# Kernel optimization log

Hardware: AMD Instinct MI355X
Metric: run time of the kernel (lower is better)

## Reference

```python
import jax, jax.numpy as jnp
import numpy as np

B, T, D, R, V = 8, 512, 1024, 4, 2048


def setup_inputs() -> dict:
    key = jax.random.key(0)
    k1, k2, k3, k4, k5 = jax.random.split(key, 5)
    return {
        "input_embs": jax.random.normal(k1, (B, T, D), dtype=jnp.float32),
        "label_ids": jax.random.randint(k2, (B, T), 0, V),
        "w_alpha": jax.random.normal(k3, (D, R), dtype=jnp.float32),
        "w_beta": jax.random.normal(k4, (D, R), dtype=jnp.float32),
        "w_vocab": jax.random.normal(k5, (D, V * R * R), dtype=jnp.float32),
    }


def _normalize(m, axis):
    # torch normalize_matrix: abs then divide by sum over `dim` (rows of the matrix)
    m = jnp.abs(m)
    return m / m.sum(axis=axis, keepdims=True)


def reference(input_embs, label_ids, w_alpha, w_beta, w_vocab):
    x = input_embs
    Bq, Tq, Dq = x.shape
    xf = x.reshape(-1, Dq)                                   # [B*T, D]
    alpha = (xf @ w_alpha).reshape(Bq, Tq, R).mean(1)        # [B, R]
    beta = (xf @ w_beta).reshape(Bq, Tq, R).mean(1)          # [B, R]
    core = (xf @ w_vocab).reshape(Bq, Tq, R, V, R).mean(1)   # [B, R, V, R]

    # gather core slices core[b, :, y[b,k], :] -> [B, T, R, R]
    g = jnp.take_along_axis(core.transpose(0, 2, 1, 3),      # [B, V, R, R]
                            label_ids[:, :, None, None], axis=1)
    Mn = _normalize(g, axis=2)                               # normalize over matrix rows (dim=0)

    v = _normalize(alpha, axis=1)                            # [B, R] normalized column vector
    Ms = Mn.transpose(1, 0, 2, 3)                            # [T, B, R, R]

    def step(v, M):
        return jnp.einsum('bij,bj->bi', M, v), None

    v, _ = jax.lax.scan(step, v, Ms)                         # sequential TT chain over T
    nb = _normalize(beta, axis=1)                            # [B, R]
    probs = jnp.einsum('bi,bi->b', nb, v)                    # [B]
    loss = -jnp.log(probs)
    return loss.mean()
```

## Files before the change

kernel.cpp:

```cpp
#include <hip/hip_runtime.h>
#include <math.h>

#define Bq 8
#define T 512
#define D 1024
#define R 4
#define V 2048
#define NCOL (V * R * R)
#define DSPLIT 16
#define DCHUNK (D / DSPLIT)
#define CBLK 1024
#define NTC 32

__global__ void k_xbar(const float* __restrict__ x, float* __restrict__ partial,
                       float* __restrict__ out) {
    int b   = blockIdx.x;
    int tc  = blockIdx.y;
    int tid = threadIdx.x;
    if (b == 0 && tc == 0 && tid == 0) out[0] = 0.f;
    const float4* xp = (const float4*)(x + ((size_t)b * T + (size_t)tc * 16) * D) + tid;
    float4 acc = make_float4(0.f, 0.f, 0.f, 0.f);
#pragma unroll
    for (int t = 0; t < 16; ++t) {
        float4 v = xp[t * (D / 4)];
        acc.x += v.x; acc.y += v.y; acc.z += v.z; acc.w += v.w;
    }
    *(float4*)(partial + ((size_t)b * NTC + tc) * D + tid * 4) = acc;
}

__global__ void k_xred(const float* __restrict__ partial, float* __restrict__ xbar) {
    int q  = blockIdx.x * 256 + threadIdx.x;
    int b  = q >> 10;
    int dd = q & 1023;
    const float* pp = partial + (size_t)b * NTC * D + dd;
    float s = 0.f;
#pragma unroll
    for (int tc = 0; tc < NTC; ++tc) s += pp[(size_t)tc * D];
    xbar[q] = s;
}

__global__ void k_core(const float* __restrict__ wv, const float* __restrict__ xbar,
                       float* __restrict__ part) {
    __shared__ float xs[Bq * DCHUNK];
    int tid  = threadIdx.x;
    int colb = blockIdx.x;
    int ds   = blockIdx.y;
    int d0   = ds * DCHUNK;

    if (tid < 128) {
        int q4 = tid * 4;
        int b  = q4 >> 6;
        int dd = q4 & 63;
        *(float4*)(xs + q4) = *(const float4*)(xbar + b * D + d0 + dd);
    }
    __syncthreads();

    int col = colb * CBLK + tid * 4;
    const float4* wp = (const float4*)(wv + (size_t)d0 * NCOL + col);
    float4 acc[Bq];
#pragma unroll
    for (int b = 0; b < Bq; ++b) acc[b] = make_float4(0.f, 0.f, 0.f, 0.f);

#pragma unroll 8
    for (int d = 0; d < DCHUNK; ++d) {
        float4 w = wp[(size_t)d * (NCOL / 4)];
#pragma unroll
        for (int b = 0; b < Bq; ++b) {
            float xv = xs[b * DCHUNK + d];
            acc[b].x += w.x * xv;
            acc[b].y += w.y * xv;
            acc[b].z += w.z * xv;
            acc[b].w += w.w * xv;
        }
    }

#pragma unroll
    for (int b = 0; b < Bq; ++b)
        *(float4*)(part + ((size_t)ds * Bq + b) * NCOL + col) = acc[b];
}

__global__ void k_gather(const float* __restrict__ part, const int* __restrict__ labels,
                         float* __restrict__ bprod) {
    __shared__ float Mn_s[64 * 16];
    __shared__ float gm[8][17];
    int b   = blockIdx.x;
    int tc  = blockIdx.y;
    int tid = threadIdx.x;
    int tl  = tid >> 2;
    int i   = tid & 3;
    int t   = tc * 64 + tl;
    int y   = labels[b * T + t];

    const float* pb = part + (size_t)b * NCOL + (size_t)i * (V * R) + (size_t)y * R;
    float4 g = make_float4(0.f, 0.f, 0.f, 0.f);
#pragma unroll
    for (int ds = 0; ds < DSPLIT; ++ds) {
        float4 v = *(const float4*)(pb + (size_t)ds * (Bq * NCOL));
        g.x += v.x; g.y += v.y; g.z += v.z; g.w += v.w;
    }
    g.x = fabsf(g.x); g.y = fabsf(g.y); g.z = fabsf(g.z); g.w = fabsf(g.w);

    float sx = g.x, sy = g.y, sz = g.z, sw = g.w;
    sx += __shfl_xor(sx, 1); sy += __shfl_xor(sy, 1);
    sz += __shfl_xor(sz, 1); sw += __shfl_xor(sw, 1);
    sx += __shfl_xor(sx, 2); sy += __shfl_xor(sy, 2);
    sz += __shfl_xor(sz, 2); sw += __shfl_xor(sw, 2);

    float4 o = make_float4(g.x / sx, g.y / sy, g.z / sz, g.w / sw);
    *(float4*)(Mn_s + tl * 16 + i * 4) = o;
    __syncthreads();

    int c = tid;
    if (c < 8) {
        const float* mp = Mn_s + c * 8 * 16;
        float P[R][R];
        {
            float4 m0 = *(const float4*)(mp + 0);
            float4 m1 = *(const float4*)(mp + 4);
            float4 m2 = *(const float4*)(mp + 8);
            float4 m3 = *(const float4*)(mp + 12);
            P[0][0]=m0.x; P[0][1]=m0.y; P[0][2]=m0.z; P[0][3]=m0.w;
            P[1][0]=m1.x; P[1][1]=m1.y; P[1][2]=m1.z; P[1][3]=m1.w;
            P[2][0]=m2.x; P[2][1]=m2.y; P[2][2]=m2.z; P[2][3]=m2.w;
            P[3][0]=m3.x; P[3][1]=m3.y; P[3][2]=m3.z; P[3][3]=m3.w;
        }
#pragma unroll
        for (int k = 1; k < 8; ++k) {
            float4 m0 = *(const float4*)(mp + k * 16 + 0);
            float4 m1 = *(const float4*)(mp + k * 16 + 4);
            float4 m2 = *(const float4*)(mp + k * 16 + 8);
            float4 m3 = *(const float4*)(mp + k * 16 + 12);
            float M[R][R] = {{m0.x, m0.y, m0.z, m0.w},
                             {m1.x, m1.y, m1.z, m1.w},
                             {m2.x, m2.y, m2.z, m2.w},
                             {m3.x, m3.y, m3.z, m3.w}};
            float N[R][R];
#pragma unroll
            for (int ii = 0; ii < R; ++ii)
#pragma unroll
                for (int j = 0; j < R; ++j)
                    N[ii][j] = M[ii][0] * P[0][j] + M[ii][1] * P[1][j] +
                               M[ii][2] * P[2][j] + M[ii][3] * P[3][j];
#pragma unroll
            for (int ii = 0; ii < R; ++ii)
#pragma unroll
                for (int j = 0; j < R; ++j) P[ii][j] = N[ii][j];
        }
#pragma unroll
        for (int ii = 0; ii < R; ++ii)
#pragma unroll
            for (int j = 0; j < R; ++j) gm[c][ii * 4 + j] = P[ii][j];
    }
    __syncthreads();

    for (int rnd = 0; rnd < 3; ++rnd) {
        int step = 1 << rnd;
        bool act = (c < 8) && ((c & (2 * step - 1)) == 0);
        float N2[R][R];
        if (act) {
            float A[R][R], Bm[R][R];
#pragma unroll
            for (int ii = 0; ii < R; ++ii)
#pragma unroll
                for (int j = 0; j < R; ++j) {
                    A[ii][j]  = gm[c + step][ii * 4 + j];
                    Bm[ii][j] = gm[c][ii * 4 + j];
                }
#pragma unroll
            for (int ii = 0; ii < R; ++ii)
#pragma unroll
                for (int j = 0; j < R; ++j)
                    N2[ii][j] = A[ii][0] * Bm[0][j] + A[ii][1] * Bm[1][j] +
                                A[ii][2] * Bm[2][j] + A[ii][3] * Bm[3][j];
        }
        __syncthreads();
        if (act) {
#pragma unroll
            for (int ii = 0; ii < R; ++ii)
#pragma unroll
                for (int j = 0; j < R; ++j) gm[c][ii * 4 + j] = N2[ii][j];
        }
        __syncthreads();
    }

    if (tid < 4)
        *(float4*)(bprod + ((size_t)(b * 8 + tc)) * 16 + tid * 4) =
            *(const float4*)(&gm[0][tid * 4]);
}

__global__ void k_chain(const float* __restrict__ bprod, const float* __restrict__ xbar,
                        const float* __restrict__ wa, const float* __restrict__ wb,
                        float* __restrict__ out) {
    __shared__ float mats[8][17];
    __shared__ float abp[64];
    int b   = blockIdx.x;
    int tid = threadIdx.x;

    {
        int r   = tid & 3;
        int sel = (tid >> 2) & 1;
        int seg = tid >> 3;
        const float* w  = sel ? wb : wa;
        const float* xp = xbar + b * D;
        float s = 0.f;
#pragma unroll 8
        for (int d = seg * 128; d < seg * 128 + 128; ++d)
            s += xp[d] * w[d * R + r];
        abp[tid] = s;
    }

    if (tid < 32) {
        int c = tid >> 2, q = tid & 3;
        *(float4*)(&mats[c][q * 4]) =
            *(const float4*)(bprod + ((size_t)(b * 8 + c)) * 16 + q * 4);
    }
    __syncthreads();

    int c = tid;
    for (int rnd = 0; rnd < 3; ++rnd) {
        int step = 1 << rnd;
        bool act = (c < 8) && ((c & (2 * step - 1)) == 0);
        float N2[R][R];
        if (act) {
            float A[R][R], Bm[R][R];
#pragma unroll
            for (int i = 0; i < R; ++i)
#pragma unroll
                for (int j = 0; j < R; ++j) {
                    A[i][j]  = mats[c + step][i * 4 + j];
                    Bm[i][j] = mats[c][i * 4 + j];
                }
#pragma unroll
            for (int i = 0; i < R; ++i)
#pragma unroll
                for (int j = 0; j < R; ++j)
                    N2[i][j] = A[i][0] * Bm[0][j] + A[i][1] * Bm[1][j] +
                               A[i][2] * Bm[2][j] + A[i][3] * Bm[3][j];
        }
        __syncthreads();
        if (act) {
#pragma unroll
            for (int i = 0; i < R; ++i)
#pragma unroll
                for (int j = 0; j < R; ++j) mats[c][i * 4 + j] = N2[i][j];
        }
        __syncthreads();
    }

    if (tid == 0) {
        float a[R], be[R];
#pragma unroll
        for (int r = 0; r < R; ++r) {
            float sa = 0.f, sb = 0.f;
#pragma unroll
            for (int seg = 0; seg < 8; ++seg) {
                sa += abp[(seg << 3) | r];
                sb += abp[(seg << 3) | 4 | r];
            }
            a[r] = sa; be[r] = sb;
        }
        float sa = fabsf(a[0]) + fabsf(a[1]) + fabsf(a[2]) + fabsf(a[3]);
        float v0[R];
#pragma unroll
        for (int r = 0; r < R; ++r) v0[r] = fabsf(a[r]) / sa;
        float v[R];
#pragma unroll
        for (int i = 0; i < R; ++i)
            v[i] = mats[0][i * 4 + 0] * v0[0] + mats[0][i * 4 + 1] * v0[1] +
                   mats[0][i * 4 + 2] * v0[2] + mats[0][i * 4 + 3] * v0[3];
        float sb = fabsf(be[0]) + fabsf(be[1]) + fabsf(be[2]) + fabsf(be[3]);
        float prob = (fabsf(be[0]) * v[0] + fabsf(be[1]) * v[1] +
                      fabsf(be[2]) * v[2] + fabsf(be[3]) * v[3]) / sb;
        atomicAdd(out, -logf(prob) * 0.125f);
    }
}

extern "C" void kernel_launch(void* const* d_in, const int* in_sizes, int n_in,
                              void* d_out, int out_size, void* d_ws, size_t ws_size,
                              hipStream_t stream) {
    const float* x      = (const float*)d_in[0];
    const int*   labels = (const int*)d_in[1];
    const float* wa     = (const float*)d_in[2];
    const float* wb     = (const float*)d_in[3];
    const float* wv     = (const float*)d_in[4];
    float* out = (float*)d_out;

    float* xbar    = (float*)d_ws;
    float* partial = xbar + Bq * D;
    float* part    = partial + (size_t)Bq * NTC * D;
    float* bprod   = part + (size_t)DSPLIT * Bq * NCOL;

    k_xbar<<<dim3(Bq, NTC), 256, 0, stream>>>(x, partial, out);
    k_xred<<<32, 256, 0, stream>>>(partial, xbar);
    k_core<<<dim3(NCOL / CBLK, DSPLIT), 256, 0, stream>>>(wv, xbar, part);
    k_gather<<<dim3(Bq, 8), 256, 0, stream>>>(part, labels, bprod);
    k_chain<<<Bq, 64, 0, stream>>>(bprod, xbar, wa, wb, out);
}
```

Before: 232.8 us.

## Fuse D-split reduction and normalization into core GEMV, drop partial buffer

Result: slower. 237.7 us (+2.1%).

```diff
diff --git a/kernel.cpp b/kernel.cpp
--- a/kernel.cpp
+++ b/kernel.cpp
@@ -7,9 +7,6 @@
 #define R 4
 #define V 2048
 #define NCOL (V * R * R)
-#define DSPLIT 16
-#define DCHUNK (D / DSPLIT)
-#define CBLK 1024
 #define NTC 32
 
 __global__ void k_xbar(const float* __restrict__ x, float* __restrict__ partial,
@@ -39,34 +36,39 @@
     xbar[q] = s;
 }
 
-__global__ void k_core(const float* __restrict__ wv, const float* __restrict__ xbar,
-                       float* __restrict__ part) {
-    __shared__ float xs[Bq * DCHUNK];
-    int tid  = threadIdx.x;
-    int colb = blockIdx.x;
-    int ds   = blockIdx.y;
-    int d0   = ds * DCHUNK;
-
-    if (tid < 128) {
-        int q4 = tid * 4;
-        int b  = q4 >> 6;
-        int dd = q4 & 63;
-        *(float4*)(xs + q4) = *(const float4*)(xbar + b * D + d0 + dd);
-    }
+__global__ void k_corey(const float* __restrict__ wv, const float* __restrict__ xbar,
+                        float* __restrict__ Mn) {
+    __shared__ float smem[10240];
+    float* xs = smem;
+
+    int tid = threadIdx.x;
+    int bid = blockIdx.x;
+    int yg  = (bid & 7) * 32 + (bid >> 3);
+
+    const float4* xb4 = (const float4*)xbar;
+#pragma unroll
+    for (int h = 0; h < 4; ++h)
+        ((float4*)xs)[h * 512 + tid] = xb4[h * 512 + tid];
     __syncthreads();
 
-    int col = colb * CBLK + tid * 4;
+    int lane = tid & 31;
+    int rg   = tid >> 5;
+    int i    = lane >> 3;
+    int seg  = lane & 7;
+    int d0   = rg * 64;
+    int col  = i * (V * R) + yg * 32 + seg * 4;
+
     const float4* wp = (const float4*)(wv + (size_t)d0 * NCOL + col);
     float4 acc[Bq];
 #pragma unroll
     for (int b = 0; b < Bq; ++b) acc[b] = make_float4(0.f, 0.f, 0.f, 0.f);
 
 #pragma unroll 8
-    for (int d = 0; d < DCHUNK; ++d) {
-        float4 w = wp[(size_t)d * (NCOL / 4)];
+    for (int dd = 0; dd < 64; ++dd) {
+        float4 w = wp[(size_t)dd * (NCOL / 4)];
 #pragma unroll
         for (int b = 0; b < Bq; ++b) {
-            float xv = xs[b * DCHUNK + d];
+            float xv = xs[b * D + d0 + dd];
             acc[b].x += w.x * xv;
             acc[b].y += w.y * xv;
             acc[b].z += w.z * xv;
@@ -74,12 +76,39 @@
         }
     }
 
-#pragma unroll
-    for (int b = 0; b < Bq; ++b)
-        *(float4*)(part + ((size_t)ds * Bq + b) * NCOL + col) = acc[b];
-}
-
-__global__ void k_gather(const float* __restrict__ part, const int* __restrict__ labels,
+    float4* red = (float4*)smem;
+#pragma unroll
+    for (int half = 0; half < 2; ++half) {
+        __syncthreads();
+#pragma unroll
+        for (int bb = 0; bb < 4; ++bb) red[tid * 5 + bb] = acc[half * 4 + bb];
+        __syncthreads();
+        if (tid < 32) {
+#pragma unroll
+            for (int bb = 0; bb < 4; ++bb) {
+                int b = half * 4 + bb;
+                float4 g = red[tid * 5 + bb];
+#pragma unroll
+                for (int r = 1; r < 16; ++r) {
+                    float4 v = red[(r * 32 + tid) * 5 + bb];
+                    g.x += v.x; g.y += v.y; g.z += v.z; g.w += v.w;
+                }
+                g.x = fabsf(g.x); g.y = fabsf(g.y);
+                g.z = fabsf(g.z); g.w = fabsf(g.w);
+                float sx = g.x, sy = g.y, sz = g.z, sw = g.w;
+                sx += __shfl_xor(sx, 8);  sy += __shfl_xor(sy, 8);
+                sz += __shfl_xor(sz, 8);  sw += __shfl_xor(sw, 8);
+                sx += __shfl_xor(sx, 16); sy += __shfl_xor(sy, 16);
+                sz += __shfl_xor(sz, 16); sw += __shfl_xor(sw, 16);
+                float4 o = make_float4(g.x / sx, g.y / sy, g.z / sz, g.w / sw);
+                int ii = tid >> 3, ss = tid & 7;
+                *(float4*)(Mn + ((size_t)b * V + yg * 8 + ss) * 16 + ii * 4) = o;
+            }
+        }
+    }
+}
+
+__global__ void k_gather(const float* __restrict__ Mn, const int* __restrict__ labels,
                          float* __restrict__ bprod) {
     __shared__ float Mn_s[64 * 16];
     __shared__ float gm[8][17];
@@ -91,22 +120,7 @@
     int t   = tc * 64 + tl;
     int y   = labels[b * T + t];
 
-    const float* pb = part + (size_t)b * NCOL + (size_t)i * (V * R) + (size_t)y * R;
-    float4 g = make_float4(0.f, 0.f, 0.f, 0.f);
-#pragma unroll
-    for (int ds = 0; ds < DSPLIT; ++ds) {
-        float4 v = *(const float4*)(pb + (size_t)ds * (Bq * NCOL));
-        g.x += v.x; g.y += v.y; g.z += v.z; g.w += v.w;
-    }
-    g.x = fabsf(g.x); g.y = fabsf(g.y); g.z = fabsf(g.z); g.w = fabsf(g.w);
-
-    float sx = g.x, sy = g.y, sz = g.z, sw = g.w;
-    sx += __shfl_xor(sx, 1); sy += __shfl_xor(sy, 1);
-    sz += __shfl_xor(sz, 1); sw += __shfl_xor(sw, 1);
-    sx += __shfl_xor(sx, 2); sy += __shfl_xor(sy, 2);
-    sz += __shfl_xor(sz, 2); sw += __shfl_xor(sw, 2);
-
-    float4 o = make_float4(g.x / sx, g.y / sy, g.z / sz, g.w / sw);
+    float4 o = *(const float4*)(Mn + ((size_t)b * V + y) * 16 + i * 4);
     *(float4*)(Mn_s + tl * 16 + i * 4) = o;
     __syncthreads();
 
@@ -287,12 +301,12 @@
 
     float* xbar    = (float*)d_ws;
     float* partial = xbar + Bq * D;
-    float* part    = partial + (size_t)Bq * NTC * D;
-    float* bprod   = part + (size_t)DSPLIT * Bq * NCOL;
+    float* Mn      = partial + (size_t)Bq * NTC * D;
+    float* bprod   = Mn + (size_t)Bq * V * 16;
 
     k_xbar<<<dim3(Bq, NTC), 256, 0, stream>>>(x, partial, out);
     k_xred<<<32, 256, 0, stream>>>(partial, xbar);
-    k_core<<<dim3(NCOL / CBLK, DSPLIT), 256, 0, stream>>>(wv, xbar, part);
-    k_gather<<<dim3(Bq, 8), 256, 0, stream>>>(part, labels, bprod);
+    k_corey<<<256, 512, 0, stream>>>(wv, xbar, Mn);
+    k_gather<<<dim3(Bq, 8), 256, 0, stream>>>(Mn, labels, bprod);
     k_chain<<<Bq, 64, 0, stream>>>(bprod, xbar, wa, wb, out);
 }
```
